# Kernel tuning notes

Hardware: AMD Instinct MI355X
Metric: run time of the kernel (lower is better)

## Reference

```python
import jax, jax.numpy as jnp
import numpy as np

B, SX, SY, C, M, OUT = 1024, 180, 130, 3, 16, 180
VR_MEAN, VR_STD, EPS = 400.0, 100.0, 1e-5
FLAT = C * SX * SY  # 70200
HID1, HID2 = 2808, OUT


def setup_inputs() -> dict:
    key = jax.random.key(0)
    ks = jax.random.split(key, 16)
    scale = 1.0 / (C * C)
    inp = {
        "x": jax.random.normal(ks[0], (B, SX, SY + 1), dtype=jnp.float32),
        # spectral weights stored as real pairs [in,out,m1,m2,2] like torch view_as_real
        "w1_0": scale * jax.random.uniform(ks[1], (C, C, M, M, 2), dtype=jnp.float32),
        "w2_0": scale * jax.random.uniform(ks[2], (C, C, M, M, 2), dtype=jnp.float32),
        "w1_1": scale * jax.random.uniform(ks[3], (C, C, M, M, 2), dtype=jnp.float32),
        "w2_1": scale * jax.random.uniform(ks[4], (C, C, M, M, 2), dtype=jnp.float32),
        "out1_w1": jax.random.normal(ks[5], (HID1, FLAT), dtype=jnp.float32) * (1.0 / np.sqrt(FLAT)),
        "out1_b1": jnp.zeros((HID1,), dtype=jnp.float32),
        "out1_w2": jax.random.normal(ks[6], (OUT, HID1), dtype=jnp.float32) * (1.0 / np.sqrt(HID1)),
        "out1_b2": jnp.zeros((OUT,), dtype=jnp.float32),
        "reg2_w1": jax.random.normal(ks[7], (OUT, 2 * OUT), dtype=jnp.float32) * (1.0 / np.sqrt(2 * OUT)),
        "reg2_b1": jnp.zeros((OUT,), dtype=jnp.float32),
        "reg2_w2": jax.random.normal(ks[8], (OUT, OUT), dtype=jnp.float32) * (1.0 / np.sqrt(OUT)),
        "reg2_b2": jnp.zeros((OUT,), dtype=jnp.float32),
    }
    return inp


def _cplx(w):
    return w[..., 0] + 1j * w[..., 1]


def _inorm(x):
    # InstanceNorm2d, affine=False: normalize each (b,c) map over spatial dims
    mu = jnp.mean(x, axis=(2, 3), keepdims=True)
    var = jnp.var(x, axis=(2, 3), keepdims=True)
    return (x - mu) * jax.lax.rsqrt(var + EPS)


def _spectral_conv(x, w1, w2):
    # x: [B,C,SX,SY]
    xft = jnp.fft.rfft2(x)  # [B,C,SX,SY//2+1]
    o1 = jnp.einsum('bixy,ioxy->boxy', xft[:, :, :M, :M], _cplx(w1))
    o2 = jnp.einsum('bixy,ioxy->boxy', xft[:, :, -M:, :M], _cplx(w2))
    out_ft = jnp.zeros(xft.shape, dtype=xft.dtype)
    out_ft = out_ft.at[:, :, :M, :M].set(o1)
    out_ft = out_ft.at[:, :, -M:, :M].set(o2)
    return jnp.fft.irfft2(out_ft, s=(SX, SY))


def reference(x, w1_0, w2_0, w1_1, w2_1, out1_w1, out1_b1, out1_w2, out1_b2,
              reg2_w1, reg2_b1, reg2_w2, reg2_b2):
    x0 = x[:, :, -1]                      # [B,180]
    h = x[:, :SX, :-1][..., None]         # [B,180,130,1]
    gx = jnp.linspace(0.0, 1.0, SX, dtype=jnp.float32)[None, :, None, None]
    gy = jnp.linspace(0.0, 1.0, SY, dtype=jnp.float32)[None, None, :, None]
    grid = jnp.concatenate([jnp.broadcast_to(gx, (x.shape[0], SX, SY, 1)),
                            jnp.broadcast_to(gy, (x.shape[0], SX, SY, 1))], axis=-1)
    h = jnp.concatenate([h, grid], axis=-1)          # [B,180,130,3]
    h = jnp.transpose(h, (0, 3, 1, 2))               # [B,3,180,130]
    h = jax.nn.gelu(_inorm(_spectral_conv(_inorm(h), w1_0, w2_0)), approximate=False)
    h = jax.nn.gelu(_inorm(_spectral_conv(_inorm(h), w1_1, w2_1)), approximate=False)
    h = h.reshape(h.shape[0], -1)                    # [B,70200]
    h = jax.nn.relu(h @ out1_w1.T + out1_b1) @ out1_w2.T + out1_b2  # [B,180]
    x0n = (x0 - VR_MEAN) / VR_STD
    # stack pred & normalized residual per output, interleave: [B,180,2] -> [B,360]
    h = jnp.stack([h, x0n], axis=-1).reshape(h.shape[0], -1)
    h = jax.nn.relu(h @ reg2_w1.T + reg2_b1) @ reg2_w2.T + reg2_b2
    return h * VR_STD + VR_MEAN
```

## Files before the change

### kernel.cpp

```cpp
#include <hip/hip_runtime.h>
#include <hip/hip_bf16.h>
#include <math.h>

#ifndef M_PI
#define M_PI 3.14159265358979323846
#endif

#define B_    1024
#define SX    180
#define SY    130
#define NC    3
#define IMG   23400
#define FLATK 70200
#define KPAD  70208
#define HID1  2808
#define NOUT  180
#define XROW  131
#define H1STR 2816
#define KSTEPS 2194
#define KCH    549

typedef __attribute__((ext_vector_type(8))) short short8;
typedef __attribute__((ext_vector_type(4))) float f32x4;
typedef __attribute__((address_space(3))) unsigned int lds_u32;
typedef __attribute__((address_space(1))) const unsigned int glb_u32;

#define TY_SH   5632
#define TX_SH   12800
#define TXI_SH  13824
#define TIY_SH  6144

__device__ __forceinline__ unsigned short f2bf(float f){
  __hip_bfloat16 h = __float2bfloat16(f);
  return __builtin_bit_cast(unsigned short, h);
}
__device__ __forceinline__ float bf2f(unsigned short u){
  __hip_bfloat16 h = __builtin_bit_cast(__hip_bfloat16, u);
  return __bfloat162float(h);
}
__device__ __forceinline__ void split_bf(float f, unsigned short &hi, unsigned short &lo){
  hi = f2bf(f);
  lo = f2bf(f - bf2f(hi));
}
__device__ __forceinline__ void gl_lds16(const void* g, void* l){
  __builtin_amdgcn_global_load_lds((glb_u32*)g, (lds_u32*)l, 16, 0, 0);
}
__device__ __forceinline__ float gelu_f(float v){
  return 0.5f * v * (1.0f + erff(v * 0.70710678118654752f));
}
__device__ __forceinline__ short8 ld_g8(const unsigned short* p){
  return *(const short8*)p;
}

__global__ void k_tables2(unsigned short* __restrict__ TyH, unsigned short* __restrict__ TyL,
                          unsigned short* __restrict__ TxH, unsigned short* __restrict__ TxL,
                          unsigned short* __restrict__ TxiH, unsigned short* __restrict__ TxiL,
                          unsigned short* __restrict__ TiyH, unsigned short* __restrict__ TiyL){
  int i = blockIdx.x*256 + threadIdx.x;
  unsigned short h, l;
  if (i < TY_SH){
    int m = i/168, y = i%168;
    float v = 0.f;
    if (m < 32 && y < SY){
      int ky = m>>1, ri = m&1;
      double ang = 2.0*M_PI*(double)((ky*y)%SY)/(double)SY;
      v = ri ? (float)(-sin(ang)) : (float)cos(ang);
    }
    split_bf(v,h,l); TyH[i]=h; TyL[i]=l;
  }
  if (i < TX_SH){
    int n = i/200, x = i%200;
    float v = 0.f;
    if (x < SX){
      int kxi = n>>1, ri = n&1;
      int kx = (kxi<16)? kxi : kxi+148;
      double ang = 2.0*M_PI*(double)((kx*x)%SX)/(double)SX;
      v = ri ? (float)sin(ang) : (float)cos(ang);
    }
    split_bf(v,h,l); TxH[i]=h; TxL[i]=l;
  }
  if (i < TXI_SH){
    int x = i/72, k = i%72;
    float v = 0.f;
    if (x < SX && k < 64){
      int kxi = k>>1, ri = k&1;
      int kx = (kxi<16)? kxi : kxi+148;
      double ang = 2.0*M_PI*(double)((kx*x)%SX)/(double)SX;
      v = (float)((ri ? sin(ang) : cos(ang)) / (double)SX);
    }
    split_bf(v,h,l); TxiH[i]=h; TxiL[i]=l;
  }
  if (i < TIY_SH){
    int y = i/40, m = i%40;
    float v = 0.f;
    if (y < SY && m < 32){
      int ky = m>>1, ri = m&1;
      if (m == 0) v = 1.0f/(float)SY;
      else if (m == 1) v = 0.f;
      else {
        double ang = 2.0*M_PI*(double)((ky*y)%SY)/(double)SY;
        v = (float)((ri ? -2.0*sin(ang) : 2.0*cos(ang)) / (double)SY);
      }
    }
    split_bf(v,h,l); TiyH[i]=h; TiyL[i]=l;
  }
}

template<int SRC>
__global__ __launch_bounds__(256) void k_fwd(const float* __restrict__ xin,
                                             const unsigned short* __restrict__ A1,
                                             const unsigned short* __restrict__ TyH,
                                             const unsigned short* __restrict__ TyL,
                                             const unsigned short* __restrict__ TxH,
                                             const unsigned short* __restrict__ TxL,
                                             float* __restrict__ Uout,
                                             float* __restrict__ Ug){
  constexpr int DHI = 0;
  constexpr int DLO = (SRC==0) ? 32256 : 0;
  constexpr int LDSN = (SRC==0) ? 64512 : 32256;
  constexpr int YTH = 0, YTL = 6400;
  __shared__ unsigned short LB[LDSN];
  __shared__ float sred[2][4];
  __shared__ float mb[2];
  int t = threadIdx.x, lane = t&63, wv = t>>6, lr = lane&15, lq = lane>>4;
  int bid = blockIdx.x;

  float s = 0.f, ss = 0.f;
  for (int i=t; i<7680; i+=256){
    int row = i/40, c4 = (i - row*40)*4;
    if (SRC == 0){
      float v[4];
      #pragma unroll
      for (int j=0;j<4;j++){
        int y = c4 + j;
        float val = 0.f;
        if (row < SX && y < SY){
          if (bid < B_)       val = xin[(size_t)bid*(SX*XROW) + row*XROW + y];
          else if (bid == B_) val = (float)row * (1.0f/179.0f);
          else                val = (float)y * (1.0f/129.0f);
        }
        s += val; ss += val*val;
        v[j] = val;
      }
      unsigned short h0,l0,h1,l1,h2,l2,h3,l3;
      split_bf(v[0],h0,l0); split_bf(v[1],h1,l1); split_bf(v[2],h2,l2); split_bf(v[3],h3,l3);
      *(ushort4*)&LB[DHI + row*168 + c4] = make_ushort4(h0,h1,h2,h3);
      *(ushort4*)&LB[DLO + row*168 + c4] = make_ushort4(l0,l1,l2,l3);
    } else {
      ushort4 d = make_ushort4(0,0,0,0);
      if (row < SX){
        const unsigned short* src = A1 + (size_t)bid*IMG + row*SY + c4;
        if (c4 <= 124){
          ushort2 a = *(const ushort2*)src;
          ushort2 b = *(const ushort2*)(src+2);
          d.x=a.x; d.y=a.y; d.z=b.x; d.w=b.y;
        } else if (c4 == 128){
          ushort2 a = *(const ushort2*)src;
          d.x=a.x; d.y=a.y;
        }
      }
      float v0=bf2f(d.x), v1=bf2f(d.y), v2=bf2f(d.z), v3=bf2f(d.w);
      s += v0+v1+v2+v3; ss += v0*v0+v1*v1+v2*v2+v3*v3;
      *(ushort4*)&LB[DHI + row*168 + c4] = d;
    }
  }
  for (int o = 32; o >= 1; o >>= 1){ s += __shfl_down(s,o); ss += __shfl_down(ss,o); }
  if (lane == 0){ sred[0][wv] = s; sred[1][wv] = ss; }
  __syncthreads();
  if (t == 0){
    float S = sred[0][0]+sred[0][1]+sred[0][2]+sred[0][3];
    float SS = sred[1][0]+sred[1][1]+sred[1][2]+sred[1][3];
    float mean = S * (1.0f/IMG);
    float var  = SS * (1.0f/IMG) - mean*mean;
    mb[0] = mean; mb[1] = rsqrtf(var + 1e-5f);
  }
  __syncthreads();

  f32x4 acc[2][3] = {};
  #pragma unroll
  for (int ks=0; ks<5; ks++){
    short8 tyh[2], tyl[2];
    #pragma unroll
    for (int mt=0; mt<2; mt++){
      tyh[mt] = ld_g8(&TyH[(mt*16+lr)*168 + ks*32 + lq*8]);
      tyl[mt] = ld_g8(&TyL[(mt*16+lr)*168 + ks*32 + lq*8]);
    }
    #pragma unroll
    for (int j=0; j<3; j++){
      int xr = (wv*3 + j)*16 + lr;
      short8 dh = *(const short8*)&LB[DHI + xr*168 + ks*32 + lq*8];
      #pragma unroll
      for (int mt=0; mt<2; mt++){
        acc[mt][j] = __builtin_amdgcn_mfma_f32_16x16x32_bf16(tyh[mt], dh, acc[mt][j], 0,0,0);
        acc[mt][j] = __builtin_amdgcn_mfma_f32_16x16x32_bf16(tyl[mt], dh, acc[mt][j], 0,0,0);
      }
      if (SRC == 0){
        short8 dl = *(const short8*)&LB[DLO + xr*168 + ks*32 + lq*8];
        #pragma unroll
        for (int mt=0; mt<2; mt++)
          acc[mt][j] = __builtin_amdgcn_mfma_f32_16x16x32_bf16(tyh[mt], dl, acc[mt][j], 0,0,0);
      }
    }
  }
  __syncthreads();

  {
    float mean = mb[0], istd = mb[1];
    #pragma unroll
    for (int mt=0; mt<2; mt++){
      #pragma unroll
      for (int j=0; j<3; j++){
        int xr = (wv*3 + j)*16 + lr;
        #pragma unroll
        for (int r=0; r<4; r++){
          int m = mt*16 + lq*4 + r;
          float v = acc[mt][j][r];
          if (m == 0) v -= 130.0f*mean;
          v *= istd;
          unsigned short h,l; split_bf(v,h,l);
          LB[YTH + m*200 + xr] = h;
          LB[YTL + m*200 + xr] = l;
        }
      }
    }
  }
  __syncthreads();

  f32x4 acc2[2] = {};
  #pragma unroll
  for (int ks=0; ks<6; ks++){
    short8 txh = ld_g8(&TxH[(wv*16+lr)*200 + ks*32 + lq*8]);
    short8 txl = ld_g8(&TxL[(wv*16+lr)*200 + ks*32 + lq*8]);
    #pragma unroll
    for (int mt=0; mt<2; mt++){
      short8 yh = *(const short8*)&LB[YTH + (mt*16+lr)*200 + ks*32 + lq*8];
      short8 yl = *(const short8*)&LB[YTL + (mt*16+lr)*200 + ks*32 + lq*8];
      acc2[mt] = __builtin_amdgcn_mfma_f32_16x16x32_bf16(yh, txh, acc2[mt], 0,0,0);
      acc2[mt] = __builtin_amdgcn_mfma_f32_16x16x32_bf16(yl, txh, acc2[mt], 0,0,0);
      acc2[mt] = __builtin_amdgcn_mfma_f32_16x16x32_bf16(yh, txl, acc2[mt], 0,0,0);
    }
  }
  float* Ub;
  if (SRC == 1) Ub = Uout + (size_t)bid*2048;
  else Ub = (bid < B_) ? (Uout + (size_t)bid*2048) : (Ug + (size_t)(bid - B_)*2048);
  #pragma unroll
  for (int mt=0; mt<2; mt++){
    #pragma unroll
    for (int r=0; r<4; r++){
      int m = mt*16 + lq*4 + r;
      int n = wv*16 + lr;
      Ub[m*64 + n] = acc2[mt][r];
    }
  }
}

template<int LAYER>
__global__ __launch_bounds__(256) void k_inv(const float* __restrict__ U1,
                                             const float* __restrict__ Ug,
                                             const float* __restrict__ U2,
                                             const float* __restrict__ w1,
                                             const float* __restrict__ w2,
                                             const unsigned short* __restrict__ TxiH,
                                             const unsigned short* __restrict__ TxiL,
                                             const unsigned short* __restrict__ TiyH,
                                             const unsigned short* __restrict__ TiyL,
                                             unsigned short* __restrict__ A1,
                                             unsigned short* __restrict__ Abf){
  constexpr int ZFH = 0;
  constexpr int ZFL = 2304;
  constexpr int GH  = 4608;
  constexpr int GL  = 12288;
  __shared__ unsigned short LB[19968];
  __shared__ float sred[2][4];
  __shared__ float mb[2];
  int t = threadIdx.x, lane = t&63, wv = t>>6, lr = lane&15, lq = lane>>4;
  int bid = blockIdx.x, b = bid/3, o = bid - b*3;

  #pragma unroll
  for (int pp=0; pp<2; pp++){
    int p = t + pp*256;
    int kxi = p & 31, ky = p >> 5;
    const float* w = (kxi < 16) ? w1 : w2;
    int kxm = kxi & 15;
    float ar = 0.f, ai = 0.f;
    #pragma unroll
    for (int i=0; i<3; i++){
      const float* Ui;
      if (LAYER == 0) Ui = (i==0) ? (U1 + (size_t)b*2048) : (Ug + (size_t)(i-1)*2048);
      else            Ui = U2 + ((size_t)b*3 + i)*2048;
      float P = Ui[(2*ky  )*64 + 2*kxi  ];
      float Q = Ui[(2*ky  )*64 + 2*kxi+1];
      float R = Ui[(2*ky+1)*64 + 2*kxi  ];
      float S = Ui[(2*ky+1)*64 + 2*kxi+1];
      float zr = P + S, zi = R - Q;
      size_t wo = ((((size_t)i*3 + o)*16 + kxm)*16 + ky)*2;
      float wr = w[wo], wi = w[wo+1];
      ar += zr*wr - zi*wi;
      ai += zr*wi + zi*wr;
    }
    unsigned short hr,lr_, hi,li, hn,ln;
    split_bf(ar,hr,lr_); split_bf(ai,hi,li); split_bf(-ai,hn,ln);
    LB[ZFH + (2*ky  )*72 + 2*kxi  ] = hr;  LB[ZFL + (2*ky  )*72 + 2*kxi  ] = lr_;
    LB[ZFH + (2*ky  )*72 + 2*kxi+1] = hn;  LB[ZFL + (2*ky  )*72 + 2*kxi+1] = ln;
    LB[ZFH + (2*ky+1)*72 + 2*kxi  ] = hi;  LB[ZFL + (2*ky+1)*72 + 2*kxi  ] = li;
    LB[ZFH + (2*ky+1)*72 + 2*kxi+1] = hr;  LB[ZFL + (2*ky+1)*72 + 2*kxi+1] = lr_;
  }
  __syncthreads();

  f32x4 acc1[2][3] = {};
  #pragma unroll
  for (int ks=0; ks<2; ks++){
    short8 zh[2], zl[2];
    #pragma unroll
    for (int mt=0; mt<2; mt++){
      zh[mt] = *(const short8*)&LB[ZFH + (mt*16+lr)*72 + ks*32 + lq*8];
      zl[mt] = *(const short8*)&LB[ZFL + (mt*16+lr)*72 + ks*32 + lq*8];
    }
    #pragma unroll
    for (int j=0; j<3; j++){
      int x = (wv*3 + j)*16 + lr;
      short8 txh = ld_g8(&TxiH[x*72 + ks*32 + lq*8]);
      short8 txl = ld_g8(&TxiL[x*72 + ks*32 + lq*8]);
      #pragma unroll
      for (int mt=0; mt<2; mt++){
        acc1[mt][j] = __builtin_amdgcn_mfma_f32_16x16x32_bf16(zh[mt], txh, acc1[mt][j], 0,0,0);
        acc1[mt][j] = __builtin_amdgcn_mfma_f32_16x16x32_bf16(zl[mt], txh, acc1[mt][j], 0,0,0);
        acc1[mt][j] = __builtin_amdgcn_mfma_f32_16x16x32_bf16(zh[mt], txl, acc1[mt][j], 0,0,0);
      }
    }
  }
  #pragma unroll
  for (int mt=0; mt<2; mt++){
    #pragma unroll
    for (int j=0; j<3; j++){
      int x = (wv*3 + j)*16 + lr;
      #pragma unroll
      for (int r=0; r<4; r++){
        int m = mt*16 + lq*4 + r;
        unsigned short h,l; split_bf(acc1[mt][j][r], h, l);
        LB[GH + x*40 + m] = h;
        LB[GL + x*40 + m] = l;
      }
    }
  }
  __syncthreads();

  f32x4 acc2[3][9] = {};
  #pragma unroll
  for (int i=0; i<3; i++){
    int x = (wv*3 + i)*16 + lr;
    short8 gh = *(const short8*)&LB[GH + x*40 + lq*8];
    short8 gl = *(const short8*)&LB[GL + x*40 + lq*8];
    #pragma unroll
    for (int yt=0; yt<9; yt++){
      short8 tyh = ld_g8(&TiyH[(yt*16+lr)*40 + lq*8]);
      short8 tyl = ld_g8(&TiyL[(yt*16+lr)*40 + lq*8]);
      acc2[i][yt] = __builtin_amdgcn_mfma_f32_16x16x32_bf16(gh, tyh, acc2[i][yt], 0,0,0);
      acc2[i][yt] = __builtin_amdgcn_mfma_f32_16x16x32_bf16(gl, tyh, acc2[i][yt], 0,0,0);
      acc2[i][yt] = __builtin_amdgcn_mfma_f32_16x16x32_bf16(gh, tyl, acc2[i][yt], 0,0,0);
    }
  }

  float s = 0.f, ss = 0.f;
  #pragma unroll
  for (int i=0; i<3; i++){
    int xt = wv*3 + i;
    #pragma unroll
    for (int yt=0; yt<9; yt++){
      #pragma unroll
      for (int r=0; r<4; r++){
        int x = xt*16 + lq*4 + r;
        int y = yt*16 + lr;
        if (x < SX && y < SY){
          float v = acc2[i][yt][r];
          s += v; ss += v*v;
        }
      }
    }
  }
  for (int off = 32; off >= 1; off >>= 1){ s += __shfl_down(s,off); ss += __shfl_down(ss,off); }
  if (lane == 0){ sred[0][wv] = s; sred[1][wv] = ss; }
  __syncthreads();
  if (t == 0){
    float S = sred[0][0]+sred[0][1]+sred[0][2]+sred[0][3];
    float SS = sred[1][0]+sred[1][1]+sred[1][2]+sred[1][3];
    float mean = S * (1.0f/IMG);
    float var  = SS * (1.0f/IMG) - mean*mean;
    mb[0] = mean; mb[1] = rsqrtf(var + 1e-5f);
  }
  __syncthreads();
  float mean = mb[0], istd = mb[1];

  unsigned short* dst = (LAYER == 0) ? (A1 + (size_t)bid*IMG)
                                     : (Abf + (size_t)b*KPAD + (size_t)o*IMG);
  #pragma unroll
  for (int i=0; i<3; i++){
    int xt = wv*3 + i;
    #pragma unroll
    for (int yt=0; yt<9; yt++){
      #pragma unroll
      for (int r=0; r<4; r++){
        int x = xt*16 + lq*4 + r;
        int y = yt*16 + lr;
        if (x < SX && y < SY){
          float v = (acc2[i][yt][r] - mean) * istd;
          dst[x*SY + y] = f2bf(gelu_f(v));
        }
      }
    }
  }
}

__global__ void k_cvt_w(const float* __restrict__ W, unsigned short* __restrict__ Wbf){
  int row = blockIdx.y;
  int gi = blockIdx.x*256 + threadIdx.x;
  if (gi >= KPAD/8) return;
  unsigned short* dst = Wbf + (size_t)row*KPAD + gi*8;
  if (gi*8 >= FLATK){
    *(ushort4*)dst = make_ushort4(0,0,0,0);
    *(ushort4*)(dst+4) = make_ushort4(0,0,0,0);
    return;
  }
  const float4* src = (const float4*)(W + (size_t)row*FLATK + gi*8);
  float4 v0 = src[0], v1 = src[1];
  ushort4 u0, u1;
  u0.x=f2bf(v0.x); u0.y=f2bf(v0.y); u0.z=f2bf(v0.z); u0.w=f2bf(v0.w);
  u1.x=f2bf(v1.x); u1.y=f2bf(v1.y); u1.z=f2bf(v1.z); u1.w=f2bf(v1.w);
  *(ushort4*)dst = u0;
  *(ushort4*)(dst+4) = u1;
}

__global__ void k_padA(unsigned short* __restrict__ Abf){
  int t = blockIdx.x*256 + threadIdx.x;
  if (t >= B_*2) return;
  int b = t >> 1, h = t & 1;
  *(ushort4*)&Abf[(size_t)b*KPAD + FLATK + h*4] = make_ushort4(0,0,0,0);
}

__global__ __launch_bounds__(256) void k_gemm_fast(const unsigned short* __restrict__ Abf,
                                                   const unsigned short* __restrict__ Wbf,
                                                   float* __restrict__ Cpart){
  __shared__ unsigned short As[2][128*32];
  __shared__ unsigned short Bs[2][128*32];
  int t = threadIdx.x;
  int lid = blockIdx.x;
  int xcd = lid & 7, inner = lid >> 3;
  int gq = inner >> 3, bx = inner & 7;
  int g = gq*8 + xcd;
  int by = g >> 2, kz = g & 3;
  int ks0 = kz*KCH, ks1 = min(ks0 + KCH, KSTEPS);
  int lane = t & 63, wv = t >> 6;
  int lr = lane & 15, lq = lane >> 4;
  int wr = wv >> 1, wc = wv & 1;
  int srow = t >> 2;
  int scol = ((t & 3) ^ ((srow >> 1) & 3)) * 8;
  const unsigned short* ga0 = Abf + (size_t)(bx*128 + srow)*KPAD + scol;
  const unsigned short* ga1 = ga0 + (size_t)64*KPAD;
  int wrow0 = min(by*128 + srow, HID1-1);
  int wrow1 = min(by*128 + 64 + srow, HID1-1);
  const unsigned short* gb0 = Wbf + (size_t)wrow0*KPAD + scol;
  const unsigned short* gb1 = Wbf + (size_t)wrow1*KPAD + scol;
  int lofs = srow*32 + (t & 3)*8;
  f32x4 acc[4][4] = {};

  {
    size_t gk = (size_t)ks0*32;
    gl_lds16(ga0 + gk, &As[0][lofs]);
    gl_lds16(ga1 + gk, &As[0][2048 + lofs]);
    gl_lds16(gb0 + gk, &Bs[0][lofs]);
    gl_lds16(gb1 + gk, &Bs[0][2048 + lofs]);
  }
  int cur = 0;
  for (int ks = ks0; ks < ks1; ks++){
    if (ks + 1 < ks1){
      size_t gk = (size_t)(ks+1)*32;
      int nb = cur ^ 1;
      gl_lds16(ga0 + gk, &As[nb][lofs]);
      gl_lds16(ga1 + gk, &As[nb][2048 + lofs]);
      gl_lds16(gb0 + gk, &Bs[nb][lofs]);
      gl_lds16(gb1 + gk, &Bs[nb][2048 + lofs]);
      asm volatile("s_waitcnt vmcnt(4)" ::: "memory");
    } else {
      asm volatile("s_waitcnt vmcnt(0)" ::: "memory");
    }
    __builtin_amdgcn_s_barrier();
    short8 a[4], b[4];
    #pragma unroll
    for (int m = 0; m < 4; m++){
      int ra = wr*64 + m*16 + lr;
      a[m] = *(const short8*)&As[cur][ra*32 + (lq ^ ((ra >> 1) & 3))*8];
    }
    #pragma unroll
    for (int n = 0; n < 4; n++){
      int rb = wc*64 + n*16 + lr;
      b[n] = *(const short8*)&Bs[cur][rb*32 + (lq ^ ((rb >> 1) & 3))*8];
    }
    #pragma unroll
    for (int m = 0; m < 4; m++){
      #pragma unroll
      for (int n = 0; n < 4; n++){
        acc[m][n] = __builtin_amdgcn_mfma_f32_16x16x32_bf16(a[m], b[n], acc[m][n], 0, 0, 0);
      }
    }
    __builtin_amdgcn_s_barrier();
    cur ^= 1;
  }
  float* Cp = Cpart + (size_t)kz*B_*H1STR;
  #pragma unroll
  for (int m = 0; m < 4; m++){
    int grow = bx*128 + wr*64 + m*16 + lq*4;
    #pragma unroll
    for (int n = 0; n < 4; n++){
      int gcol = by*128 + wc*64 + n*16 + lr;
      #pragma unroll
      for (int r = 0; r < 4; r++)
        Cp[(size_t)(grow + r)*H1STR + gcol] = acc[m][n][r];
    }
  }
}

__global__ void k_red(const float* __restrict__ Cp, const float* __restrict__ bias,
                      float* __restrict__ h1){
  size_t idx = (size_t)(blockIdx.x*256 + threadIdx.x)*4;
  if (idx >= (size_t)B_*H1STR) return;
  int col = (int)(idx % H1STR);
  float4 a = *(const float4*)(Cp + idx);
  float4 b = *(const float4*)(Cp + (size_t)B_*H1STR + idx);
  float4 c = *(const float4*)(Cp + (size_t)2*B_*H1STR + idx);
  float4 d = *(const float4*)(Cp + (size_t)3*B_*H1STR + idx);
  float4 o;
  o.x = fmaxf(a.x+b.x+c.x+d.x + ((col+0)<HID1 ? bias[col+0] : 0.f), 0.f);
  o.y = fmaxf(a.y+b.y+c.y+d.y + ((col+1)<HID1 ? bias[col+1] : 0.f), 0.f);
  o.z = fmaxf(a.z+b.z+c.z+d.z + ((col+2)<HID1 ? bias[col+2] : 0.f), 0.f);
  o.w = fmaxf(a.w+b.w+c.w+d.w + ((col+3)<HID1 ? bias[col+3] : 0.f), 0.f);
  *(float4*)(h1 + idx) = o;
}

__global__ __launch_bounds__(256) void k_gemm2(const float* __restrict__ h1,
                                               const float* __restrict__ w2,
                                               const float* __restrict__ b2,
                                               float* __restrict__ o1){
  __shared__ float hs[16][68];
  __shared__ float wsm[16][68];
  int t = threadIdx.x;
  int bx = blockIdx.x, by = blockIdx.y;
  int r = t >> 4, c4 = (t & 15) * 4;
  int bi = t >> 4, oi = t & 15;
  float acc = 0.f;
  for (int ks = 0; ks < 44; ks++){
    int gk = ks*64 + c4;
    float4 va = make_float4(0.f,0.f,0.f,0.f);
    if (gk < HID1) va = *(const float4*)&h1[(size_t)(bx*16 + r)*H1STR + gk];
    *(float4*)&hs[r][c4] = va;
    int go = by*16 + r;
    float4 vb = make_float4(0.f,0.f,0.f,0.f);
    if (gk < HID1 && go < NOUT) vb = *(const float4*)&w2[(size_t)go*HID1 + gk];
    *(float4*)&wsm[r][c4] = vb;
    __syncthreads();
    #pragma unroll 8
    for (int k = 0; k < 64; k++) acc += hs[bi][k] * wsm[oi][k];
    __syncthreads();
  }
  int go = by*16 + oi;
  if (go < NOUT) o1[(size_t)(bx*16 + bi)*NOUT + go] = acc + b2[go];
}

__global__ void k_reg2(const float* __restrict__ o1, const float* __restrict__ xin,
                       const float* __restrict__ w1, const float* __restrict__ b1,
                       const float* __restrict__ w2, const float* __restrict__ b2,
                       float* __restrict__ outp){
  __shared__ float s[360];
  __shared__ float tt[180];
  int b = blockIdx.x, t = threadIdx.x;
  if (t < 180){
    s[2*t]   = o1[b*NOUT + t];
    s[2*t+1] = (xin[(size_t)b*SX*XROW + t*XROW + (XROW-1)] - 400.0f) * 0.01f;
  }
  __syncthreads();
  if (t < 180){
    float a = b1[t];
    for (int j = 0; j < 360; j++) a += s[j] * w1[t*360 + j];
    tt[t] = fmaxf(a, 0.0f);
  }
  __syncthreads();
  if (t < 180){
    float a = b2[t];
    for (int j = 0; j < 180; j++) a += tt[j] * w2[t*180 + j];
    outp[b*NOUT + t] = a*100.0f + 400.0f;
  }
}

extern "C" void kernel_launch(void* const* d_in, const int* in_sizes, int n_in,
                              void* d_out, int out_size, void* d_ws, size_t ws_size,
                              hipStream_t stream){
  const float* xin   = (const float*)d_in[0];
  const float* wA0   = (const float*)d_in[1];
  const float* wB0   = (const float*)d_in[2];
  const float* wA1   = (const float*)d_in[3];
  const float* wB1   = (const float*)d_in[4];
  const float* o1w1  = (const float*)d_in[5];
  const float* o1b1  = (const float*)d_in[6];
  const float* o1w2  = (const float*)d_in[7];
  const float* o1b2  = (const float*)d_in[8];
  const float* r2w1  = (const float*)d_in[9];
  const float* r2b1  = (const float*)d_in[10];
  const float* r2w2  = (const float*)d_in[11];
  const float* r2b2  = (const float*)d_in[12];
  float* ws  = (float*)d_ws;
  float* out = (float*)d_out;

  unsigned short* tab = (unsigned short*)ws;
  unsigned short *TyH = tab,            *TyL = tab + TY_SH;
  unsigned short *TxH = TyL + TY_SH,    *TxL = TxH + TX_SH;
  unsigned short *TxiH = TxL + TX_SH,   *TxiL = TxiH + TXI_SH;
  unsigned short *TiyH = TxiL + TXI_SH, *TiyL = TiyH + TIY_SH;

  size_t oU1  = 38400;
  size_t oUg  = oU1  + (size_t)B_*2048;
  size_t oU2  = oUg  + 4096;
  size_t oA1  = oU2  + (size_t)3072*2048;
  size_t oAbf = oA1  + (size_t)3072*IMG/2;
  size_t oWbf = oAbf + (size_t)B_*KPAD/2;
  size_t oCp  = oWbf + (size_t)HID1*KPAD/2;
  size_t oH1  = oCp  + (size_t)4*B_*H1STR;
  size_t oO1  = oH1  + (size_t)B_*H1STR;

  float *U1 = ws + oU1, *Ug = ws + oUg, *U2 = ws + oU2;
  unsigned short *A1  = (unsigned short*)(ws + oA1);
  unsigned short *Abf = (unsigned short*)(ws + oAbf);
  unsigned short *Wbf = (unsigned short*)(ws + oWbf);
  float *Cpart = ws + oCp, *H1 = ws + oH1, *O1 = ws + oO1;

  k_tables2<<<54, 256, 0, stream>>>(TyH, TyL, TxH, TxL, TxiH, TxiL, TiyH, TiyL);

  k_fwd<0><<<B_ + 2, 256, 0, stream>>>(xin, nullptr, TyH, TyL, TxH, TxL, U1, Ug);
  k_inv<0><<<3072, 256, 0, stream>>>(U1, Ug, nullptr, wA0, wB0, TxiH, TxiL, TiyH, TiyL, A1, nullptr);
  k_fwd<1><<<3072, 256, 0, stream>>>(nullptr, A1, TyH, TyL, TxH, TxL, U2, nullptr);
  k_inv<1><<<3072, 256, 0, stream>>>(nullptr, nullptr, U2, wA1, wB1, TxiH, TxiL, TiyH, TiyL, nullptr, Abf);

  k_padA<<<8, 256, 0, stream>>>(Abf);
  k_cvt_w<<<dim3(35, HID1), 256, 0, stream>>>(o1w1, Wbf);
  k_gemm_fast<<<704, 256, 0, stream>>>(Abf, Wbf, Cpart);
  k_red<<<(B_*H1STR/4 + 255)/256, 256, 0, stream>>>(Cpart, o1b1, H1);
  k_gemm2<<<dim3(64, 12), 256, 0, stream>>>(H1, o1w2, o1b2, O1);
  k_reg2<<<B_, 192, 0, stream>>>(O1, xin, r2w1, r2b1, r2w2, r2b2, out);
}
```

Before: 1.320 ms.

## Fuse layer-0 inverse FFT with layer-1 forward FFT; raise GEMM split-K to 8

```diff
diff --git a/kernel.cpp b/kernel.cpp
--- a/kernel.cpp
+++ b/kernel.cpp
@@ -18,7 +18,8 @@
 #define XROW  131
 #define H1STR 2816
 #define KSTEPS 2194
-#define KCH    549
+#define KCH8   275
+#define NKZ    8
 
 typedef __attribute__((ext_vector_type(8))) short short8;
 typedef __attribute__((ext_vector_type(4))) float f32x4;
@@ -106,20 +107,16 @@
   }
 }
 
-template<int SRC>
-__global__ __launch_bounds__(256) void k_fwd(const float* __restrict__ xin,
-                                             const unsigned short* __restrict__ A1,
-                                             const unsigned short* __restrict__ TyH,
-                                             const unsigned short* __restrict__ TyL,
-                                             const unsigned short* __restrict__ TxH,
-                                             const unsigned short* __restrict__ TxL,
-                                             float* __restrict__ Uout,
-                                             float* __restrict__ Ug){
+__global__ __launch_bounds__(256) void k_fwd0(const float* __restrict__ xin,
+                                              const unsigned short* __restrict__ TyH,
+                                              const unsigned short* __restrict__ TyL,
+                                              const unsigned short* __restrict__ TxH,
+                                              const unsigned short* __restrict__ TxL,
+                                              float* __restrict__ U1,
+                                              float* __restrict__ Ug){
   constexpr int DHI = 0;
-  constexpr int DLO = (SRC==0) ? 32256 : 0;
-  constexpr int LDSN = (SRC==0) ? 64512 : 32256;
   constexpr int YTH = 0, YTL = 6400;
-  __shared__ unsigned short LB[LDSN];
+  __shared__ unsigned short LB[32256];
   __shared__ float sred[2][4];
   __shared__ float mb[2];
   int t = threadIdx.x, lane = t&63, wv = t>>6, lr = lane&15, lq = lane>>4;
@@ -128,41 +125,21 @@
   float s = 0.f, ss = 0.f;
   for (int i=t; i<7680; i+=256){
     int row = i/40, c4 = (i - row*40)*4;
-    if (SRC == 0){
-      float v[4];
-      #pragma unroll
-      for (int j=0;j<4;j++){
-        int y = c4 + j;
-        float val = 0.f;
-        if (row < SX && y < SY){
-          if (bid < B_)       val = xin[(size_t)bid*(SX*XROW) + row*XROW + y];
-          else if (bid == B_) val = (float)row * (1.0f/179.0f);
-          else                val = (float)y * (1.0f/129.0f);
-        }
-        s += val; ss += val*val;
-        v[j] = val;
-      }
-      unsigned short h0,l0,h1,l1,h2,l2,h3,l3;
-      split_bf(v[0],h0,l0); split_bf(v[1],h1,l1); split_bf(v[2],h2,l2); split_bf(v[3],h3,l3);
-      *(ushort4*)&LB[DHI + row*168 + c4] = make_ushort4(h0,h1,h2,h3);
-      *(ushort4*)&LB[DLO + row*168 + c4] = make_ushort4(l0,l1,l2,l3);
-    } else {
-      ushort4 d = make_ushort4(0,0,0,0);
-      if (row < SX){
-        const unsigned short* src = A1 + (size_t)bid*IMG + row*SY + c4;
-        if (c4 <= 124){
-          ushort2 a = *(const ushort2*)src;
-          ushort2 b = *(const ushort2*)(src+2);
-          d.x=a.x; d.y=a.y; d.z=b.x; d.w=b.y;
-        } else if (c4 == 128){
-          ushort2 a = *(const ushort2*)src;
-          d.x=a.x; d.y=a.y;
-        }
-      }
-      float v0=bf2f(d.x), v1=bf2f(d.y), v2=bf2f(d.z), v3=bf2f(d.w);
-      s += v0+v1+v2+v3; ss += v0*v0+v1*v1+v2*v2+v3*v3;
-      *(ushort4*)&LB[DHI + row*168 + c4] = d;
-    }
+    float v[4];
+    #pragma unroll
+    for (int j=0;j<4;j++){
+      int y = c4 + j;
+      float val = 0.f;
+      if (row < SX && y < SY){
+        if (bid < B_)       val = xin[(size_t)bid*(SX*XROW) + row*XROW + y];
+        else if (bid == B_) val = (float)row * (1.0f/179.0f);
+        else                val = (float)y * (1.0f/129.0f);
+      }
+      s += val; ss += val*val;
+      v[j] = val;
+    }
+    ushort4 u; u.x=f2bf(v[0]); u.y=f2bf(v[1]); u.z=f2bf(v[2]); u.w=f2bf(v[3]);
+    *(ushort4*)&LB[DHI + row*168 + c4] = u;
   }
   for (int o = 32; o >= 1; o >>= 1){ s += __shfl_down(s,o); ss += __shfl_down(ss,o); }
   if (lane == 0){ sred[0][wv] = s; sred[1][wv] = ss; }
@@ -193,12 +170,6 @@
       for (int mt=0; mt<2; mt++){
         acc[mt][j] = __builtin_amdgcn_mfma_f32_16x16x32_bf16(tyh[mt], dh, acc[mt][j], 0,0,0);
         acc[mt][j] = __builtin_amdgcn_mfma_f32_16x16x32_bf16(tyl[mt], dh, acc[mt][j], 0,0,0);
-      }
-      if (SRC == 0){
-        short8 dl = *(const short8*)&LB[DLO + xr*168 + ks*32 + lq*8];
-        #pragma unroll
-        for (int mt=0; mt<2; mt++)
-          acc[mt][j] = __builtin_amdgcn_mfma_f32_16x16x32_bf16(tyh[mt], dl, acc[mt][j], 0,0,0);
       }
     }
   }
@@ -240,9 +211,7 @@
       acc2[mt] = __builtin_amdgcn_mfma_f32_16x16x32_bf16(yh, txl, acc2[mt], 0,0,0);
     }
   }
-  float* Ub;
-  if (SRC == 1) Ub = Uout + (size_t)bid*2048;
-  else Ub = (bid < B_) ? (Uout + (size_t)bid*2048) : (Ug + (size_t)(bid - B_)*2048);
+  float* Ub = (bid < B_) ? (U1 + (size_t)bid*2048) : (Ug + (size_t)(bid - B_)*2048);
   #pragma unroll
   for (int mt=0; mt<2; mt++){
     #pragma unroll
@@ -254,23 +223,23 @@
   }
 }
 
-template<int LAYER>
-__global__ __launch_bounds__(256) void k_inv(const float* __restrict__ U1,
+__global__ __launch_bounds__(256) void k_mid(const float* __restrict__ U1,
                                              const float* __restrict__ Ug,
-                                             const float* __restrict__ U2,
                                              const float* __restrict__ w1,
                                              const float* __restrict__ w2,
                                              const unsigned short* __restrict__ TxiH,
                                              const unsigned short* __restrict__ TxiL,
                                              const unsigned short* __restrict__ TiyH,
                                              const unsigned short* __restrict__ TiyL,
-                                             unsigned short* __restrict__ A1,
-                                             unsigned short* __restrict__ Abf){
-  constexpr int ZFH = 0;
-  constexpr int ZFL = 2304;
-  constexpr int GH  = 4608;
-  constexpr int GL  = 12288;
-  __shared__ unsigned short LB[19968];
+                                             const unsigned short* __restrict__ TyH,
+                                             const unsigned short* __restrict__ TyL,
+                                             const unsigned short* __restrict__ TxH,
+                                             const unsigned short* __restrict__ TxL,
+                                             float* __restrict__ U2){
+  constexpr int ZFH = 0, ZFL = 2304, GH = 4608, GL = 12288;
+  constexpr int DAT = 0;
+  constexpr int YTH = 0, YTL = 6400;
+  __shared__ unsigned short LB[32256];
   __shared__ float sred[2][4];
   __shared__ float mb[2];
   int t = threadIdx.x, lane = t&63, wv = t>>6, lr = lane&15, lq = lane>>4;
@@ -285,9 +254,7 @@
     float ar = 0.f, ai = 0.f;
     #pragma unroll
     for (int i=0; i<3; i++){
-      const float* Ui;
-      if (LAYER == 0) Ui = (i==0) ? (U1 + (size_t)b*2048) : (Ug + (size_t)(i-1)*2048);
-      else            Ui = U2 + ((size_t)b*3 + i)*2048;
+      const float* Ui = (i==0) ? (U1 + (size_t)b*2048) : (Ug + (size_t)(i-1)*2048);
       float P = Ui[(2*ky  )*64 + 2*kxi  ];
       float Q = Ui[(2*ky  )*64 + 2*kxi+1];
       float R = Ui[(2*ky+1)*64 + 2*kxi  ];
@@ -389,10 +356,256 @@
     mb[0] = mean; mb[1] = rsqrtf(var + 1e-5f);
   }
   __syncthreads();
+  float mean1 = mb[0], istd1 = mb[1];
+
+  for (int i=t; i<8064; i+=256)
+    *(ushort4*)&LB[DAT + i*4] = make_ushort4(0,0,0,0);
+  float s2 = 0.f, ss2 = 0.f;
+  #pragma unroll
+  for (int i=0; i<3; i++){
+    int xt = wv*3 + i;
+    #pragma unroll
+    for (int yt=0; yt<9; yt++){
+      #pragma unroll
+      for (int r=0; r<4; r++){
+        int x = xt*16 + lq*4 + r;
+        int y = yt*16 + lr;
+        float d = 0.f;
+        if (x < SX && y < SY){
+          d = gelu_f((acc2[i][yt][r] - mean1) * istd1);
+          s2 += d; ss2 += d*d;
+        }
+        acc2[i][yt][r] = d;
+      }
+    }
+  }
+  for (int off = 32; off >= 1; off >>= 1){ s2 += __shfl_down(s2,off); ss2 += __shfl_down(ss2,off); }
+  if (lane == 0){ sred[0][wv] = s2; sred[1][wv] = ss2; }
+  __syncthreads();
+  if (t == 0){
+    float S = sred[0][0]+sred[0][1]+sred[0][2]+sred[0][3];
+    float SS = sred[1][0]+sred[1][1]+sred[1][2]+sred[1][3];
+    float mean = S * (1.0f/IMG);
+    float var  = SS * (1.0f/IMG) - mean*mean;
+    mb[0] = mean; mb[1] = rsqrtf(var + 1e-5f);
+  }
+  __syncthreads();
+
+  #pragma unroll
+  for (int i=0; i<3; i++){
+    int xt = wv*3 + i;
+    #pragma unroll
+    for (int yt=0; yt<9; yt++){
+      #pragma unroll
+      for (int r=0; r<4; r++){
+        int x = xt*16 + lq*4 + r;
+        int y = yt*16 + lr;
+        if (x < SX && y < SY)
+          LB[DAT + x*168 + y] = f2bf(acc2[i][yt][r]);
+      }
+    }
+  }
+  __syncthreads();
+
+  f32x4 accf[2][3] = {};
+  #pragma unroll
+  for (int ks=0; ks<5; ks++){
+    short8 tyh[2], tyl[2];
+    #pragma unroll
+    for (int mt=0; mt<2; mt++){
+      tyh[mt] = ld_g8(&TyH[(mt*16+lr)*168 + ks*32 + lq*8]);
+      tyl[mt] = ld_g8(&TyL[(mt*16+lr)*168 + ks*32 + lq*8]);
+    }
+    #pragma unroll
+    for (int j=0; j<3; j++){
+      int xr = (wv*3 + j)*16 + lr;
+      short8 dh = *(const short8*)&LB[DAT + xr*168 + ks*32 + lq*8];
+      #pragma unroll
+      for (int mt=0; mt<2; mt++){
+        accf[mt][j] = __builtin_amdgcn_mfma_f32_16x16x32_bf16(tyh[mt], dh, accf[mt][j], 0,0,0);
+        accf[mt][j] = __builtin_amdgcn_mfma_f32_16x16x32_bf16(tyl[mt], dh, accf[mt][j], 0,0,0);
+      }
+    }
+  }
+  __syncthreads();
+
+  {
+    float mean2 = mb[0], istd2 = mb[1];
+    #pragma unroll
+    for (int mt=0; mt<2; mt++){
+      #pragma unroll
+      for (int j=0; j<3; j++){
+        int xr = (wv*3 + j)*16 + lr;
+        #pragma unroll
+        for (int r=0; r<4; r++){
+          int m = mt*16 + lq*4 + r;
+          float v = accf[mt][j][r];
+          if (m == 0) v -= 130.0f*mean2;
+          v *= istd2;
+          unsigned short h,l; split_bf(v,h,l);
+          LB[YTH + m*200 + xr] = h;
+          LB[YTL + m*200 + xr] = l;
+        }
+      }
+    }
+  }
+  __syncthreads();
+
+  f32x4 accu[2] = {};
+  #pragma unroll
+  for (int ks=0; ks<6; ks++){
+    short8 txh = ld_g8(&TxH[(wv*16+lr)*200 + ks*32 + lq*8]);
+    short8 txl = ld_g8(&TxL[(wv*16+lr)*200 + ks*32 + lq*8]);
+    #pragma unroll
+    for (int mt=0; mt<2; mt++){
+      short8 yh = *(const short8*)&LB[YTH + (mt*16+lr)*200 + ks*32 + lq*8];
+      short8 yl = *(const short8*)&LB[YTL + (mt*16+lr)*200 + ks*32 + lq*8];
+      accu[mt] = __builtin_amdgcn_mfma_f32_16x16x32_bf16(yh, txh, accu[mt], 0,0,0);
+      accu[mt] = __builtin_amdgcn_mfma_f32_16x16x32_bf16(yl, txh, accu[mt], 0,0,0);
+      accu[mt] = __builtin_amdgcn_mfma_f32_16x16x32_bf16(yh, txl, accu[mt], 0,0,0);
+    }
+  }
+  float* Ub = U2 + (size_t)bid*2048;
+  #pragma unroll
+  for (int mt=0; mt<2; mt++){
+    #pragma unroll
+    for (int r=0; r<4; r++){
+      int m = mt*16 + lq*4 + r;
+      int n = wv*16 + lr;
+      Ub[m*64 + n] = accu[mt][r];
+    }
+  }
+}
+
+__global__ __launch_bounds__(256) void k_inv1(const float* __restrict__ U2,
+                                              const float* __restrict__ w1,
+                                              const float* __restrict__ w2,
+                                              const unsigned short* __restrict__ TxiH,
+                                              const unsigned short* __restrict__ TxiL,
+                                              const unsigned short* __restrict__ TiyH,
+                                              const unsigned short* __restrict__ TiyL,
+                                              unsigned short* __restrict__ Abf){
+  constexpr int ZFH = 0, ZFL = 2304, GH = 4608, GL = 12288;
+  __shared__ unsigned short LB[19968];
+  __shared__ float sred[2][4];
+  __shared__ float mb[2];
+  int t = threadIdx.x, lane = t&63, wv = t>>6, lr = lane&15, lq = lane>>4;
+  int bid = blockIdx.x, b = bid/3, o = bid - b*3;
+
+  #pragma unroll
+  for (int pp=0; pp<2; pp++){
+    int p = t + pp*256;
+    int kxi = p & 31, ky = p >> 5;
+    const float* w = (kxi < 16) ? w1 : w2;
+    int kxm = kxi & 15;
+    float ar = 0.f, ai = 0.f;
+    #pragma unroll
+    for (int i=0; i<3; i++){
+      const float* Ui = U2 + ((size_t)b*3 + i)*2048;
+      float P = Ui[(2*ky  )*64 + 2*kxi  ];
+      float Q = Ui[(2*ky  )*64 + 2*kxi+1];
+      float R = Ui[(2*ky+1)*64 + 2*kxi  ];
+      float S = Ui[(2*ky+1)*64 + 2*kxi+1];
+      float zr = P + S, zi = R - Q;
+      size_t wo = ((((size_t)i*3 + o)*16 + kxm)*16 + ky)*2;
+      float wr = w[wo], wi = w[wo+1];
+      ar += zr*wr - zi*wi;
+      ai += zr*wi + zi*wr;
+    }
+    unsigned short hr,lr_, hi,li, hn,ln;
+    split_bf(ar,hr,lr_); split_bf(ai,hi,li); split_bf(-ai,hn,ln);
+    LB[ZFH + (2*ky  )*72 + 2*kxi  ] = hr;  LB[ZFL + (2*ky  )*72 + 2*kxi  ] = lr_;
+    LB[ZFH + (2*ky  )*72 + 2*kxi+1] = hn;  LB[ZFL + (2*ky  )*72 + 2*kxi+1] = ln;
+    LB[ZFH + (2*ky+1)*72 + 2*kxi  ] = hi;  LB[ZFL + (2*ky+1)*72 + 2*kxi  ] = li;
+    LB[ZFH + (2*ky+1)*72 + 2*kxi+1] = hr;  LB[ZFL + (2*ky+1)*72 + 2*kxi+1] = lr_;
+  }
+  __syncthreads();
+
+  f32x4 acc1[2][3] = {};
+  #pragma unroll
+  for (int ks=0; ks<2; ks++){
+    short8 zh[2], zl[2];
+    #pragma unroll
+    for (int mt=0; mt<2; mt++){
+      zh[mt] = *(const short8*)&LB[ZFH + (mt*16+lr)*72 + ks*32 + lq*8];
+      zl[mt] = *(const short8*)&LB[ZFL + (mt*16+lr)*72 + ks*32 + lq*8];
+    }
+    #pragma unroll
+    for (int j=0; j<3; j++){
+      int x = (wv*3 + j)*16 + lr;
+      short8 txh = ld_g8(&TxiH[x*72 + ks*32 + lq*8]);
+      short8 txl = ld_g8(&TxiL[x*72 + ks*32 + lq*8]);
+      #pragma unroll
+      for (int mt=0; mt<2; mt++){
+        acc1[mt][j] = __builtin_amdgcn_mfma_f32_16x16x32_bf16(zh[mt], txh, acc1[mt][j], 0,0,0);
+        acc1[mt][j] = __builtin_amdgcn_mfma_f32_16x16x32_bf16(zl[mt], txh, acc1[mt][j], 0,0,0);
+        acc1[mt][j] = __builtin_amdgcn_mfma_f32_16x16x32_bf16(zh[mt], txl, acc1[mt][j], 0,0,0);
+      }
+    }
+  }
+  #pragma unroll
+  for (int mt=0; mt<2; mt++){
+    #pragma unroll
+    for (int j=0; j<3; j++){
+      int x = (wv*3 + j)*16 + lr;
+      #pragma unroll
+      for (int r=0; r<4; r++){
+        int m = mt*16 + lq*4 + r;
+        unsigned short h,l; split_bf(acc1[mt][j][r], h, l);
+        LB[GH + x*40 + m] = h;
+        LB[GL + x*40 + m] = l;
+      }
+    }
+  }
+  __syncthreads();
+
+  f32x4 acc2[3][9] = {};
+  #pragma unroll
+  for (int i=0; i<3; i++){
+    int x = (wv*3 + i)*16 + lr;
+    short8 gh = *(const short8*)&LB[GH + x*40 + lq*8];
+    short8 gl = *(const short8*)&LB[GL + x*40 + lq*8];
+    #pragma unroll
+    for (int yt=0; yt<9; yt++){
+      short8 tyh = ld_g8(&TiyH[(yt*16+lr)*40 + lq*8]);
+      short8 tyl = ld_g8(&TiyL[(yt*16+lr)*40 + lq*8]);
+      acc2[i][yt] = __builtin_amdgcn_mfma_f32_16x16x32_bf16(gh, tyh, acc2[i][yt], 0,0,0);
+      acc2[i][yt] = __builtin_amdgcn_mfma_f32_16x16x32_bf16(gl, tyh, acc2[i][yt], 0,0,0);
+      acc2[i][yt] = __builtin_amdgcn_mfma_f32_16x16x32_bf16(gh, tyl, acc2[i][yt], 0,0,0);
+    }
+  }
+
+  float s = 0.f, ss = 0.f;
+  #pragma unroll
+  for (int i=0; i<3; i++){
+    int xt = wv*3 + i;
+    #pragma unroll
+    for (int yt=0; yt<9; yt++){
+      #pragma unroll
+      for (int r=0; r<4; r++){
+        int x = xt*16 + lq*4 + r;
+        int y = yt*16 + lr;
+        if (x < SX && y < SY){
+          float v = acc2[i][yt][r];
+          s += v; ss += v*v;
+        }
+      }
+    }
+  }
+  for (int off = 32; off >= 1; off >>= 1){ s += __shfl_down(s,off); ss += __shfl_down(ss,off); }
+  if (lane == 0){ sred[0][wv] = s; sred[1][wv] = ss; }
+  __syncthreads();
+  if (t == 0){
+    float S = sred[0][0]+sred[0][1]+sred[0][2]+sred[0][3];
+    float SS = sred[1][0]+sred[1][1]+sred[1][2]+sred[1][3];
+    float mean = S * (1.0f/IMG);
+    float var  = SS * (1.0f/IMG) - mean*mean;
+    mb[0] = mean; mb[1] = rsqrtf(var + 1e-5f);
+  }
+  __syncthreads();
   float mean = mb[0], istd = mb[1];
 
-  unsigned short* dst = (LAYER == 0) ? (A1 + (size_t)bid*IMG)
-                                     : (Abf + (size_t)b*KPAD + (size_t)o*IMG);
+  unsigned short* dst = Abf + (size_t)b*KPAD + (size_t)o*IMG;
   #pragma unroll
   for (int i=0; i<3; i++){
     int xt = wv*3 + i;
@@ -447,8 +660,8 @@
   int xcd = lid & 7, inner = lid >> 3;
   int gq = inner >> 3, bx = inner & 7;
   int g = gq*8 + xcd;
-  int by = g >> 2, kz = g & 3;
-  int ks0 = kz*KCH, ks1 = min(ks0 + KCH, KSTEPS);
+  int by = g >> 3, kz = g & 7;
+  int ks0 = kz*KCH8, ks1 = min(ks0 + KCH8, KSTEPS);
   int lane = t & 63, wv = t >> 6;
   int lr = lane & 15, lq = lane >> 4;
   int wr = wv >> 1, wc = wv & 1;
@@ -524,15 +737,17 @@
   size_t idx = (size_t)(blockIdx.x*256 + threadIdx.x)*4;
   if (idx >= (size_t)B_*H1STR) return;
   int col = (int)(idx % H1STR);
-  float4 a = *(const float4*)(Cp + idx);
-  float4 b = *(const float4*)(Cp + (size_t)B_*H1STR + idx);
-  float4 c = *(const float4*)(Cp + (size_t)2*B_*H1STR + idx);
-  float4 d = *(const float4*)(Cp + (size_t)3*B_*H1STR + idx);
+  float4 acc = make_float4(0.f,0.f,0.f,0.f);
+  #pragma unroll
+  for (int j = 0; j < NKZ; j++){
+    float4 v = *(const float4*)(Cp + (size_t)j*B_*H1STR + idx);
+    acc.x += v.x; acc.y += v.y; acc.z += v.z; acc.w += v.w;
+  }
   float4 o;
-  o.x = fmaxf(a.x+b.x+c.x+d.x + ((col+0)<HID1 ? bias[col+0] : 0.f), 0.f);
-  o.y = fmaxf(a.y+b.y+c.y+d.y + ((col+1)<HID1 ? bias[col+1] : 0.f), 0.f);
-  o.z = fmaxf(a.z+b.z+c.z+d.z + ((col+2)<HID1 ? bias[col+2] : 0.f), 0.f);
-  o.w = fmaxf(a.w+b.w+c.w+d.w + ((col+3)<HID1 ? bias[col+3] : 0.f), 0.f);
+  o.x = fmaxf(acc.x + ((col+0)<HID1 ? bias[col+0] : 0.f), 0.f);
+  o.y = fmaxf(acc.y + ((col+1)<HID1 ? bias[col+1] : 0.f), 0.f);
+  o.z = fmaxf(acc.z + ((col+2)<HID1 ? bias[col+2] : 0.f), 0.f);
+  o.w = fmaxf(acc.w + ((col+3)<HID1 ? bias[col+3] : 0.f), 0.f);
   *(float4*)(h1 + idx) = o;
 }
 
@@ -618,29 +833,27 @@
   size_t oU1  = 38400;
   size_t oUg  = oU1  + (size_t)B_*2048;
   size_t oU2  = oUg  + 4096;
-  size_t oA1  = oU2  + (size_t)3072*2048;
-  size_t oAbf = oA1  + (size_t)3072*IMG/2;
+  size_t oAbf = oU2  + (size_t)3072*2048;
   size_t oWbf = oAbf + (size_t)B_*KPAD/2;
   size_t oCp  = oWbf + (size_t)HID1*KPAD/2;
-  size_t oH1  = oCp  + (size_t)4*B_*H1STR;
+  size_t oH1  = oCp  + (size_t)NKZ*B_*H1STR;
   size_t oO1  = oH1  + (size_t)B_*H1STR;
 
   float *U1 = ws + oU1, *Ug = ws + oUg, *U2 = ws + oU2;
-  unsigned short *A1  = (unsigned short*)(ws + oA1);
   unsigned short *Abf = (unsigned short*)(ws + oAbf);
   unsigned short *Wbf = (unsigned short*)(ws + oWbf);
   float *Cpart = ws + oCp, *H1 = ws + oH1, *O1 = ws + oO1;
 
   k_tables2<<<54, 256, 0, stream>>>(TyH, TyL, TxH, TxL, TxiH, TxiL, TiyH, TiyL);
 
-  k_fwd<0><<<B_ + 2, 256, 0, stream>>>(xin, nullptr, TyH, TyL, TxH, TxL, U1, Ug);
-  k_inv<0><<<3072, 256, 0, stream>>>(U1, Ug, nullptr, wA0, wB0, TxiH, TxiL, TiyH, TiyL, A1, nullptr);
-  k_fwd<1><<<3072, 256, 0, stream>>>(nullptr, A1, TyH, TyL, TxH, TxL, U2, nullptr);
-  k_inv<1><<<3072, 256, 0, stream>>>(nullptr, nullptr, U2, wA1, wB1, TxiH, TxiL, TiyH, TiyL, nullptr, Abf);
+  k_fwd0<<<B_ + 2, 256, 0, stream>>>(xin, TyH, TyL, TxH, TxL, U1, Ug);
+  k_mid<<<3072, 256, 0, stream>>>(U1, Ug, wA0, wB0, TxiH, TxiL, TiyH, TiyL,
+                                  TyH, TyL, TxH, TxL, U2);
+  k_inv1<<<3072, 256, 0, stream>>>(U2, wA1, wB1, TxiH, TxiL, TiyH, TiyL, Abf);
 
   k_padA<<<8, 256, 0, stream>>>(Abf);
   k_cvt_w<<<dim3(35, HID1), 256, 0, stream>>>(o1w1, Wbf);
-  k_gemm_fast<<<704, 256, 0, stream>>>(Abf, Wbf, Cpart);
+  k_gemm_fast<<<1408, 256, 0, stream>>>(Abf, Wbf, Cpart);
   k_red<<<(B_*H1STR/4 + 255)/256, 256, 0, stream>>>(Cpart, o1b1, H1);
   k_gemm2<<<dim3(64, 12), 256, 0, stream>>>(H1, o1w2, o1b2, O1);
   k_reg2<<<B_, 192, 0, stream>>>(O1, xin, r2w1, r2b1, r2w2, r2b2, out);
```

After: 1.238 ms. 1.07x faster.
